# Kernel optimization log

Hardware: AMD Instinct MI355X
Metric: run time of the kernel (lower is better)

Reference implementation:

```python
import jax, jax.numpy as jnp
import numpy as np

N, E, F_IN, F_E, L = 10000, 50000, 40, 10, 64

def setup_inputs() -> dict:
    key = jax.random.key(0)
    ks = jax.random.split(key, 12)
    f32 = jnp.float32
    def rn(k, shape, s=0.1):
        return jax.random.normal(k, shape, dtype=f32) * s
    return {
        "x": rn(ks[0], (N, F_IN), 1.0),
        "edge_index": jax.random.randint(ks[1], (2, E), 0, N),
        "edge_attr": rn(ks[2], (E, F_E), 1.0),
        "lin0_w": rn(ks[3], (F_IN, L)), "lin0_b": jnp.zeros((L,), f32),
        "nn1_w": rn(ks[4], (F_E, L)), "nn1_b": jnp.zeros((L,), f32),
        "nn2_w": rn(ks[5], (L, L * L), 0.02), "nn2_b": jnp.zeros((L * L,), f32),
        "conv_root": rn(ks[6], (L, L)), "conv_bias": jnp.zeros((L,), f32),
        "gru_w_ih": rn(ks[7], (L, 3 * L)), "gru_w_hh": rn(ks[8], (L, 3 * L)),
        "gru_b_ih": jnp.zeros((3 * L,), f32), "gru_b_hh": jnp.zeros((3 * L,), f32),
        "lin1_w": rn(ks[9], (L, L)), "lin1_b": jnp.zeros((L,), f32),
        "lin2_w": rn(ks[10], (L, 1)), "lin2_b": jnp.zeros((1,), f32),
    }

def reference(x, edge_index, edge_attr, lin0_w, lin0_b, nn1_w, nn1_b,
              nn2_w, nn2_b, conv_root, conv_bias, gru_w_ih, gru_w_hh,
              gru_b_ih, gru_b_hh, lin1_w, lin1_b, lin2_w, lin2_b):
    n = x.shape[0]
    l = lin0_b.shape[0]
    src, dst = edge_index[0], edge_index[1]

    # mean-aggregation normalization (nodes with no in-edges -> 0)
    deg = jax.ops.segment_sum(jnp.ones_like(edge_attr[:, 0]), dst, num_segments=n)
    inv_deg = (1.0 / jnp.maximum(deg, 1.0))[:, None]  # [N,1]

    # edge-conditioned weights: nnet(edge_attr).view(E, L, L) -- edge_attr is
    # loop-invariant so compute once (same math as recomputing each iter)
    w_edge = (jax.nn.relu(edge_attr @ nn1_w + nn1_b) @ nn2_w + nn2_b).reshape(-1, l, l)

    out = jax.nn.relu(x @ lin0_w + lin0_b)  # [N,L]
    h = out
    for _ in range(3):
        # NNConv: gather src feats, per-edge matvec, scatter-mean, + root + bias
        msg = jnp.einsum('ei,eio->eo', out[src], w_edge)  # [E,L]
        agg = jax.ops.segment_sum(msg, dst, num_segments=n) * inv_deg
        m = jax.nn.relu(agg + out @ conv_root + conv_bias)
        # single-step GRU (torch nn.GRU equations)
        gi = m @ gru_w_ih + gru_b_ih
        gh = h @ gru_w_hh + gru_b_hh
        r = jax.nn.sigmoid(gi[:, :l] + gh[:, :l])
        z = jax.nn.sigmoid(gi[:, l:2 * l] + gh[:, l:2 * l])
        ng = jnp.tanh(gi[:, 2 * l:] + r * gh[:, 2 * l:])
        h = (1.0 - z) * ng + z * h
        out = h

    out = jax.nn.relu(out @ lin1_w + lin1_b)
    return out @ lin2_w + lin2_b  # [N,1]
```

## Files before the change

### kernel.cpp

```cpp
#include <hip/hip_runtime.h>
#include <hip/hip_bf16.h>

#define NN 10000
#define NP 10016
#define NE 50000
#define FIN 40
#define FE 10
#define MCH 20

typedef float f32x4 __attribute__((ext_vector_type(4)));
typedef short s16x8 __attribute__((ext_vector_type(8)));

__device__ __forceinline__ float bcast(float v, int lane) {
    return __uint_as_float(__builtin_amdgcn_readlane(__float_as_uint(v), lane));
}
__device__ __forceinline__ int bcast_i(int v, int lane) {
    return __builtin_amdgcn_readlane(v, lane);
}
__device__ __forceinline__ ushort f2bf(float f) {
    uint u = __float_as_uint(f);
    uint r = (u + 0x7FFFu + ((u >> 16) & 1u)) >> 16;
    return (ushort)r;
}
__device__ __forceinline__ float bf2f(ushort h) {
    return __uint_as_float(((uint)h) << 16);
}

__global__ void k_count(const int* __restrict__ ei, int* __restrict__ deg) {
    int e = blockIdx.x * 256 + threadIdx.x;
    if (e < NE) atomicAdd(&deg[ei[NE + e]], 1);
}

__global__ __launch_bounds__(1024) void k_scan(const int* __restrict__ deg,
                                               int* __restrict__ rowp,
                                               int* __restrict__ fill,
                                               float* __restrict__ invd) {
    __shared__ int wsum[16];
    __shared__ int chunkbase;
    int tid = threadIdx.x, lane = tid & 63, wv = tid >> 6;
    if (tid == 0) chunkbase = 0;
    __syncthreads();
    for (int base = 0; base < NN; base += 1024) {
        int idx = base + tid;
        int v = (idx < NN) ? deg[idx] : 0;
        int s = v;
#pragma unroll
        for (int off = 1; off < 64; off <<= 1) {
            int t = __shfl_up(s, off, 64);
            if (lane >= off) s += t;
        }
        if (lane == 63) wsum[wv] = s;
        __syncthreads();
        int carry = chunkbase;
        if (wv == 0 && lane < 16) {
            int x = wsum[lane];
#pragma unroll
            for (int off = 1; off < 16; off <<= 1) {
                int t = __shfl_up(x, off, 64);
                if (lane >= off) x += t;
            }
            wsum[lane] = x;
        }
        __syncthreads();
        int wpre = (wv == 0) ? 0 : wsum[wv - 1];
        int incl = carry + wpre + s;
        if (idx < NN) {
            rowp[idx] = incl - v;
            fill[idx] = incl - v;
            invd[idx] = 1.0f / (float)(v > 0 ? v : 1);
        }
        __syncthreads();
        if (tid == 0) chunkbase = carry + wsum[15];
        __syncthreads();
    }
    if (tid == 0) rowp[NN] = NE;
}

__global__ void k_fill(const int* __restrict__ ei, int* __restrict__ fill,
                       int* __restrict__ csrs, int* __restrict__ csre) {
    int e = blockIdx.x * 256 + threadIdx.x;
    if (e < NE) {
        int d = ei[NE + e];
        int p = atomicAdd(&fill[d], 1);
        csrs[p] = ei[e];
        csre[p] = e;
    }
}

__global__ __launch_bounds__(256) void k_w2f(const float* __restrict__ n2w,
                                             ushort* __restrict__ W2FH,
                                             ushort* __restrict__ W2FL) {
    int lane = threadIdx.x & 63, wvl = threadIdx.x >> 6;
    int ki = blockIdx.x * 4 + wvl;
    float v = n2w[(size_t)ki * 64 + lane];
    ushort hi = f2bf(v);
    ushort lo = f2bf(v - bf2f(hi));
    W2FH[(size_t)lane * 4096 + ki] = hi;
    W2FL[(size_t)lane * 4096 + ki] = lo;
}

__global__ __launch_bounds__(256) void k_edge_h(const float* __restrict__ ea,
                                                const float* __restrict__ w1,
                                                const float* __restrict__ b1,
                                                float* __restrict__ hE) {
    int lane = threadIdx.x & 63, wv = threadIdx.x >> 6;
    int e = blockIdx.x * 4 + wv;
    float av = (lane < FE) ? ea[e * FE + lane] : 0.f;
    float acc = b1[lane];
#pragma unroll
    for (int j = 0; j < FE; ++j) acc += bcast(av, j) * w1[j * 64 + lane];
    hE[e * 64 + lane] = fmaxf(acc, 0.f);
}

__global__ __launch_bounds__(256) void k_lin0(const float* __restrict__ x,
                                              const float* __restrict__ w0,
                                              const float* __restrict__ b0,
                                              float* __restrict__ F) {
    int lane = threadIdx.x & 63, wv = threadIdx.x >> 6;
    int n = blockIdx.x * 4 + wv;
    float xv = (lane < FIN) ? x[n * FIN + lane] : 0.f;
    float acc = b0[lane];
#pragma unroll
    for (int k = 0; k < FIN; ++k) acc += bcast(xv, k) * w0[k * 64 + lane];
    F[n * 64 + lane] = fmaxf(acc, 0.f);
}

__global__ __launch_bounds__(256) void k_gather(
    const float* __restrict__ F, const float* __restrict__ hE,
    const int* __restrict__ rowp, const int* __restrict__ csrs,
    const int* __restrict__ csre,
    ushort* __restrict__ GH, float* __restrict__ Usb) {
    int tid = threadIdx.x, lane = tid & 63, wv = tid >> 6;
    int n = __builtin_amdgcn_readfirstlane(blockIdx.x * 4 + wv);
    int beg = __builtin_amdgcn_readfirstlane(rowp[n]);
    int end = __builtin_amdgcn_readfirstlane(rowp[n + 1]);

    float G[64];
#pragma unroll
    for (int k = 0; k < 64; ++k) G[k] = 0.f;
    float usum = 0.f;
    {
        int p0 = beg + lane;
        int sl = (p0 < end) ? csrs[p0] : 0;
        int el = (p0 < end) ? csre[p0] : 0;
        int nb = min(end - beg, 64);
        for (int j = 0; j < nb; ++j) {
            int s = bcast_i(sl, j);
            int e = bcast_i(el, j);
            float u = F[(size_t)s * 64 + lane];
            float hv = hE[(size_t)e * 64 + lane];
            usum += u;
#pragma unroll
            for (int k = 0; k < 64; ++k) G[k] = fmaf(bcast(hv, k), u, G[k]);
        }
        for (int p = beg + 64; p < end; ++p) {
            int s = __builtin_amdgcn_readfirstlane(csrs[p]);
            int e = __builtin_amdgcn_readfirstlane(csre[p]);
            float u = F[(size_t)s * 64 + lane];
            float hv = hE[(size_t)e * 64 + lane];
            usum += u;
#pragma unroll
            for (int k = 0; k < 64; ++k) G[k] = fmaf(bcast(hv, k), u, G[k]);
        }
    }
    Usb[(size_t)n * 64 + lane] = usum;
    ushort* gout = GH + (size_t)n * 4096 + lane;
#pragma unroll
    for (int k = 0; k < 64; ++k) gout[k * 64] = f2bf(G[k]);
}

__global__ __launch_bounds__(512) void k_contract(
    const ushort* __restrict__ GH, const ushort* __restrict__ W2FH,
    const ushort* __restrict__ W2FL, float* __restrict__ AggP) {
    __shared__ __align__(16) ushort BH[64 * 520];
    __shared__ __align__(16) ushort BL[64 * 520];
    int tid = threadIdx.x, lane = tid & 63, wv = tid >> 6;
    int ks = blockIdx.x & 7;
    int mc = blockIdx.x >> 3;
    int kbase = ks * 512;
    int otile = wv & 3, mhalf = wv >> 2;
    int arow = lane & 15, agrp = lane >> 4;
    int o = otile * 16 + arow;

#pragma unroll
    for (int rep = 0; rep < 8; ++rep) {
        int off = rep * 4096 + tid * 8;
        int row = off >> 9, col = off & 511;
        *(s16x8*)&BH[row * 520 + col] =
            *(const s16x8*)&W2FH[(size_t)row * 4096 + kbase + col];
        *(s16x8*)&BL[row * 520 + col] =
            *(const s16x8*)&W2FL[(size_t)row * 4096 + kbase + col];
    }
    __syncthreads();

    int mg0 = mc * MCH;
    int mgend = min(mg0 + MCH, NP / 16);
    float* ap = AggP + (size_t)ks * NN * 64;
    for (int mg = mg0 + mhalf * 2; mg < mgend; mg += 4) {
        const ushort* pA = GH + (size_t)(mg * 16 + arow) * 4096 + kbase;
        const ushort* pB = GH + (size_t)((mg + 1) * 16 + arow) * 4096 + kbase;
        f32x4 acc0 = {0.f, 0.f, 0.f, 0.f};
        f32x4 acc1 = {0.f, 0.f, 0.f, 0.f};
#pragma unroll 4
        for (int s = 0; s < 16; ++s) {
            int kil = s * 32 + agrp * 8;
            s16x8 a0 = *(const s16x8*)&pA[kil];
            s16x8 a1 = *(const s16x8*)&pB[kil];
            s16x8 bh = *(const s16x8*)&BH[o * 520 + kil];
            s16x8 bl = *(const s16x8*)&BL[o * 520 + kil];
            acc0 = __builtin_amdgcn_mfma_f32_16x16x32_bf16(a0, bh, acc0, 0, 0, 0);
            acc1 = __builtin_amdgcn_mfma_f32_16x16x32_bf16(a1, bh, acc1, 0, 0, 0);
            acc0 = __builtin_amdgcn_mfma_f32_16x16x32_bf16(a0, bl, acc0, 0, 0, 0);
            acc1 = __builtin_amdgcn_mfma_f32_16x16x32_bf16(a1, bl, acc1, 0, 0, 0);
        }
#pragma unroll
        for (int r = 0; r < 4; ++r) {
            int n0r = mg * 16 + agrp * 4 + r;
            if (n0r < NN) ap[(size_t)n0r * 64 + o] = acc0[r];
            int n1r = (mg + 1) * 16 + agrp * 4 + r;
            if (n1r < NN) ap[(size_t)n1r * 64 + o] = acc1[r];
        }
    }
}

__global__ __launch_bounds__(256) void k_epi(
    const float* __restrict__ AggP, const float* __restrict__ Usb,
    const float* __restrict__ B2, const float* __restrict__ invd,
    const float* __restrict__ F, const float* __restrict__ Wroot,
    const float* __restrict__ broot, const float* __restrict__ Wih,
    const float* __restrict__ Whh, const float* __restrict__ bih,
    const float* __restrict__ bhh, float* __restrict__ Fout) {
    int lane = threadIdx.x & 63, wv = threadIdx.x >> 6;
    int nq = blockIdx.x * 16 + wv * 4;

    float fv[4], uv[4], aa[4], rt[4], bt[4];
#pragma unroll
    for (int q = 0; q < 4; ++q) {
        size_t idx = (size_t)(nq + q) * 64 + lane;
        fv[q] = F[idx];
        uv[q] = Usb[idx];
        float s = 0.f;
#pragma unroll
        for (int ks = 0; ks < 8; ++ks) s += AggP[(size_t)ks * NN * 64 + idx];
        aa[q] = s;
        rt[q] = broot[lane];
        bt[q] = 0.f;
    }
#pragma unroll 8
    for (int k = 0; k < 64; ++k) {
        float wr = Wroot[k * 64 + lane];
        float b2 = B2[k * 64 + lane];
#pragma unroll
        for (int q = 0; q < 4; ++q) {
            rt[q] = fmaf(bcast(fv[q], k), wr, rt[q]);
            bt[q] = fmaf(bcast(uv[q], k), b2, bt[q]);
        }
    }
    float m[4];
#pragma unroll
    for (int q = 0; q < 4; ++q)
        m[q] = fmaxf((aa[q] + bt[q]) * invd[nq + q] + rt[q], 0.f);

    float sr[4], sz[4], gn[4], gh[4];
#pragma unroll
    for (int q = 0; q < 4; ++q) {
        sr[q] = bih[lane] + bhh[lane];
        sz[q] = bih[64 + lane] + bhh[64 + lane];
        gn[q] = bih[128 + lane];
        gh[q] = bhh[128 + lane];
    }
#pragma unroll 8
    for (int k = 0; k < 64; ++k) {
        float wi0 = Wih[k * 192 + lane];
        float wi1 = Wih[k * 192 + 64 + lane];
        float wi2 = Wih[k * 192 + 128 + lane];
        float wh0 = Whh[k * 192 + lane];
        float wh1 = Whh[k * 192 + 64 + lane];
        float wh2 = Whh[k * 192 + 128 + lane];
#pragma unroll
        for (int q = 0; q < 4; ++q) {
            float mk = bcast(m[q], k), hk = bcast(fv[q], k);
            sr[q] = fmaf(mk, wi0, fmaf(hk, wh0, sr[q]));
            sz[q] = fmaf(mk, wi1, fmaf(hk, wh1, sz[q]));
            gn[q] = fmaf(mk, wi2, gn[q]);
            gh[q] = fmaf(hk, wh2, gh[q]);
        }
    }
#pragma unroll
    for (int q = 0; q < 4; ++q) {
        float rr = 1.f / (1.f + __expf(-sr[q]));
        float zz = 1.f / (1.f + __expf(-sz[q]));
        float ng = tanhf(gn[q] + rr * gh[q]);
        Fout[(size_t)(nq + q) * 64 + lane] = (1.f - zz) * ng + zz * fv[q];
    }
}

__global__ __launch_bounds__(256) void k_final(const float* __restrict__ F,
                                               const float* __restrict__ W1,
                                               const float* __restrict__ b1f,
                                               const float* __restrict__ W2l,
                                               const float* __restrict__ b2f,
                                               float* __restrict__ out) {
    int lane = threadIdx.x & 63, wv = threadIdx.x >> 6;
    int n = blockIdx.x * 4 + wv;
    float fv = F[n * 64 + lane];
    float acc = b1f[lane];
#pragma unroll
    for (int k = 0; k < 64; ++k) acc += bcast(fv, k) * W1[k * 64 + lane];
    acc = fmaxf(acc, 0.f);
    float p = acc * W2l[lane];
#pragma unroll
    for (int off = 32; off; off >>= 1) p += __shfl_xor(p, off, 64);
    if (lane == 0) out[n] = p + b2f[0];
}

extern "C" void kernel_launch(void* const* d_in, const int* in_sizes, int n_in,
                              void* d_out, int out_size, void* d_ws, size_t ws_size,
                              hipStream_t stream) {
    const float* x = (const float*)d_in[0];
    const int* ei = (const int*)d_in[1];
    const float* ea = (const float*)d_in[2];
    const float* l0w = (const float*)d_in[3];
    const float* l0b = (const float*)d_in[4];
    const float* n1w = (const float*)d_in[5];
    const float* n1b = (const float*)d_in[6];
    const float* n2w = (const float*)d_in[7];
    const float* n2b = (const float*)d_in[8];
    const float* cr = (const float*)d_in[9];
    const float* cb = (const float*)d_in[10];
    const float* wih = (const float*)d_in[11];
    const float* whh = (const float*)d_in[12];
    const float* bih = (const float*)d_in[13];
    const float* bhh = (const float*)d_in[14];
    const float* l1w = (const float*)d_in[15];
    const float* l1b = (const float*)d_in[16];
    const float* l2w = (const float*)d_in[17];
    const float* l2b = (const float*)d_in[18];

    char* w = (char*)d_ws;
    size_t off = 0;
    float* F0 = (float*)(w + off); off += (size_t)NN * 64 * 4;
    float* F1 = (float*)(w + off); off += (size_t)NN * 64 * 4;
    float* hE = (float*)(w + off); off += (size_t)NE * 64 * 4;
    ushort* W2FH = (ushort*)(w + off); off += (size_t)64 * 4096 * 2;
    ushort* W2FL = (ushort*)(w + off); off += (size_t)64 * 4096 * 2;
    ushort* GH = (ushort*)(w + off); off += (size_t)NP * 4096 * 2;
    float* AggP = (float*)(w + off); off += (size_t)8 * NN * 64 * 4;
    float* Usb = (float*)(w + off); off += (size_t)NN * 64 * 4;
    float* invd = (float*)(w + off); off += (size_t)NN * 4;
    int* deg = (int*)(w + off); off += (size_t)NN * 4;
    int* rowp = (int*)(w + off); off += (size_t)(NN + 1) * 4 + 252; off &= ~(size_t)255;
    int* fill = (int*)(w + off); off += (size_t)NN * 4;
    int* csrs = (int*)(w + off); off += (size_t)NE * 4;
    int* csre = (int*)(w + off); off += (size_t)NE * 4;

    hipMemsetAsync(deg, 0, NN * 4, stream);
    k_count<<<(NE + 255) / 256, 256, 0, stream>>>(ei, deg);
    k_scan<<<1, 1024, 0, stream>>>(deg, rowp, fill, invd);
    k_fill<<<(NE + 255) / 256, 256, 0, stream>>>(ei, fill, csrs, csre);
    k_w2f<<<1024, 256, 0, stream>>>(n2w, W2FH, W2FL);
    k_edge_h<<<NE / 4, 256, 0, stream>>>(ea, n1w, n1b, hE);
    k_lin0<<<NN / 4, 256, 0, stream>>>(x, l0w, l0b, F0);
    float* Fcur = F0;
    float* Fnxt = F1;
    for (int it = 0; it < 3; ++it) {
        k_gather<<<NN / 4, 256, 0, stream>>>(Fcur, hE, rowp, csrs, csre, GH, Usb);
        k_contract<<<32 * 8, 512, 0, stream>>>(GH, W2FH, W2FL, AggP);
        k_epi<<<NN / 16, 256, 0, stream>>>(AggP, Usb, n2b, invd, Fcur, cr, cb,
                                           wih, whh, bih, bhh, Fnxt);
        float* t = Fcur; Fcur = Fnxt; Fnxt = t;
    }
    k_final<<<NN / 4, 256, 0, stream>>>(Fcur, l1w, l1b, l2w, l2b, (float*)d_out);
}
```

Before: 323.1 us.

## Split contract kernel over output halves to double grid and halve LDS

The contraction kernel now splits the 64 output columns across two blocks, so the grid doubles to 512 blocks and each block stages only 32 rows of the hi/lo weight tiles in shared memory. Waves are remapped to 2 output tiles by 4 row groups. The hi and lo bf16 products go into separate accumulators that are summed at the end, which shortens the MFMA dependency chains. NP is padded to 10240 so every chunk is full and the bound check can be dropped. The cost is that each GH A-tile is now read by two blocks instead of one, doubling that global traffic.

```diff
diff --git a/kernel.cpp b/kernel.cpp
--- a/kernel.cpp
+++ b/kernel.cpp
@@ -2,7 +2,7 @@
 #include <hip/hip_bf16.h>
 
 #define NN 10000
-#define NP 10016
+#define NP 10240
 #define NE 50000
 #define FIN 40
 #define FE 10
@@ -172,47 +172,53 @@
 __global__ __launch_bounds__(512) void k_contract(
     const ushort* __restrict__ GH, const ushort* __restrict__ W2FH,
     const ushort* __restrict__ W2FL, float* __restrict__ AggP) {
-    __shared__ __align__(16) ushort BH[64 * 520];
-    __shared__ __align__(16) ushort BL[64 * 520];
+    __shared__ __align__(16) ushort BH[32 * 520];
+    __shared__ __align__(16) ushort BL[32 * 520];
     int tid = threadIdx.x, lane = tid & 63, wv = tid >> 6;
-    int ks = blockIdx.x & 7;
-    int mc = blockIdx.x >> 3;
+    int oh = blockIdx.x & 1;
+    int ks = (blockIdx.x >> 1) & 7;
+    int mc = blockIdx.x >> 4;
     int kbase = ks * 512;
-    int otile = wv & 3, mhalf = wv >> 2;
+    int otile = wv & 1, mq = wv >> 1;
     int arow = lane & 15, agrp = lane >> 4;
-    int o = otile * 16 + arow;
-
-#pragma unroll
-    for (int rep = 0; rep < 8; ++rep) {
+    int lr = otile * 16 + arow;
+    int o = oh * 32 + lr;
+
+#pragma unroll
+    for (int rep = 0; rep < 4; ++rep) {
         int off = rep * 4096 + tid * 8;
         int row = off >> 9, col = off & 511;
         *(s16x8*)&BH[row * 520 + col] =
-            *(const s16x8*)&W2FH[(size_t)row * 4096 + kbase + col];
+            *(const s16x8*)&W2FH[(size_t)(oh * 32 + row) * 4096 + kbase + col];
         *(s16x8*)&BL[row * 520 + col] =
-            *(const s16x8*)&W2FL[(size_t)row * 4096 + kbase + col];
+            *(const s16x8*)&W2FL[(size_t)(oh * 32 + row) * 4096 + kbase + col];
     }
     __syncthreads();
 
     int mg0 = mc * MCH;
-    int mgend = min(mg0 + MCH, NP / 16);
+    int mgend = mg0 + MCH;
     float* ap = AggP + (size_t)ks * NN * 64;
-    for (int mg = mg0 + mhalf * 2; mg < mgend; mg += 4) {
+    for (int mg = mg0 + mq * 2; mg < mgend; mg += 8) {
         const ushort* pA = GH + (size_t)(mg * 16 + arow) * 4096 + kbase;
         const ushort* pB = GH + (size_t)((mg + 1) * 16 + arow) * 4096 + kbase;
-        f32x4 acc0 = {0.f, 0.f, 0.f, 0.f};
-        f32x4 acc1 = {0.f, 0.f, 0.f, 0.f};
+        f32x4 a0h = {0.f, 0.f, 0.f, 0.f};
+        f32x4 a0l = {0.f, 0.f, 0.f, 0.f};
+        f32x4 a1h = {0.f, 0.f, 0.f, 0.f};
+        f32x4 a1l = {0.f, 0.f, 0.f, 0.f};
 #pragma unroll 4
         for (int s = 0; s < 16; ++s) {
             int kil = s * 32 + agrp * 8;
             s16x8 a0 = *(const s16x8*)&pA[kil];
             s16x8 a1 = *(const s16x8*)&pB[kil];
-            s16x8 bh = *(const s16x8*)&BH[o * 520 + kil];
-            s16x8 bl = *(const s16x8*)&BL[o * 520 + kil];
-            acc0 = __builtin_amdgcn_mfma_f32_16x16x32_bf16(a0, bh, acc0, 0, 0, 0);
-            acc1 = __builtin_amdgcn_mfma_f32_16x16x32_bf16(a1, bh, acc1, 0, 0, 0);
-            acc0 = __builtin_amdgcn_mfma_f32_16x16x32_bf16(a0, bl, acc0, 0, 0, 0);
-            acc1 = __builtin_amdgcn_mfma_f32_16x16x32_bf16(a1, bl, acc1, 0, 0, 0);
-        }
+            s16x8 bh = *(const s16x8*)&BH[lr * 520 + kil];
+            s16x8 bl = *(const s16x8*)&BL[lr * 520 + kil];
+            a0h = __builtin_amdgcn_mfma_f32_16x16x32_bf16(a0, bh, a0h, 0, 0, 0);
+            a1h = __builtin_amdgcn_mfma_f32_16x16x32_bf16(a1, bh, a1h, 0, 0, 0);
+            a0l = __builtin_amdgcn_mfma_f32_16x16x32_bf16(a0, bl, a0l, 0, 0, 0);
+            a1l = __builtin_amdgcn_mfma_f32_16x16x32_bf16(a1, bl, a1l, 0, 0, 0);
+        }
+        f32x4 acc0 = a0h + a0l;
+        f32x4 acc1 = a1h + a1l;
 #pragma unroll
         for (int r = 0; r < 4; ++r) {
             int n0r = mg * 16 + agrp * 4 + r;
@@ -365,7 +371,7 @@
     float* Fnxt = F1;
     for (int it = 0; it < 3; ++it) {
         k_gather<<<NN / 4, 256, 0, stream>>>(Fcur, hE, rowp, csrs, csre, GH, Usb);
-        k_contract<<<32 * 8, 512, 0, stream>>>(GH, W2FH, W2FL, AggP);
+        k_contract<<<512, 512, 0, stream>>>(GH, W2FH, W2FL, AggP);
         k_epi<<<NN / 16, 256, 0, stream>>>(AggP, Usb, n2b, invd, Fcur, cr, cb,
                                            wih, whh, bih, bhh, Fnxt);
         float* t = Fcur; Fcur = Fnxt; Fnxt = t;
```

After: 322.0 us. About the same (-0.3%).
